# Kernel optimization log

Measured on AMD Instinct MI355X. Metric: run time of the kernel, lower is better.

Reference implementation:

```python
import jax, jax.numpy as jnp
import numpy as np

LAYERS, BLOCKS = 10, 4
RC, DC, SC, EC = 32, 32, 256, 256  # residual, dilation, skip, end channels
CIN, COUT, K = 6, 1, 2
DILATIONS = [2 ** (i % LAYERS) for i in range(BLOCKS * LAYERS)]
NL = len(DILATIONS)


def conv1d(x, w, dilation=1, pad=0):
    # x: [N, C, T], w: [O, I, K]
    return jax.lax.conv_general_dilated(
        x, w, window_strides=(1,), padding=[(pad, pad)],
        rhs_dilation=(dilation,), dimension_numbers=('NCH', 'OIH', 'NCH'))


def setup_inputs() -> dict:
    key = jax.random.key(0)
    ks = jax.random.split(key, 10)
    s = 0.1
    return {
        'x': jax.random.normal(ks[0], (8, CIN, 8192), dtype=jnp.float32),
        'start_w': jax.random.normal(ks[1], (RC, CIN, 1), dtype=jnp.float32) * s,
        'filter_w': jax.random.normal(ks[2], (NL, DC, RC, K), dtype=jnp.float32) * s,
        'gate_w': jax.random.normal(ks[3], (NL, DC, RC, K), dtype=jnp.float32) * s,
        'res_w': jax.random.normal(ks[4], (NL, RC, DC, 1), dtype=jnp.float32) * s,
        'skip_w': jax.random.normal(ks[5], (NL, SC, DC, 1), dtype=jnp.float32) * s,
        'end1_w': jax.random.normal(ks[6], (EC, SC, 1), dtype=jnp.float32) * s,
        'end1_b': jax.random.normal(ks[7], (EC,), dtype=jnp.float32) * s,
        'end2_w': jax.random.normal(ks[8], (COUT, EC, 1), dtype=jnp.float32) * s,
        'end2_b': jax.random.normal(ks[9], (COUT,), dtype=jnp.float32) * s,
    }


def reference(x, start_w, filter_w, gate_w, res_w, skip_w, end1_w, end1_b, end2_w, end2_b):
    x = conv1d(x, start_w)  # [B, RC, T]
    T = x.shape[2]
    # symmetric padding=(K-1)*d makes length grow by d each layer;
    # the shortest skip is the first one: T + (K-1)*DILATIONS[0]
    min_len = T + (K - 1) * DILATIONS[0]
    skip_sum = jnp.zeros((x.shape[0], SC, min_len), dtype=x.dtype)
    for i, d in enumerate(DILATIONS):
        pad = (K - 1) * d
        f = jnp.tanh(conv1d(x, filter_w[i], d, pad))
        g = jax.nn.sigmoid(conv1d(x, gate_w[i], d, pad))
        x = f * g  # [B, DC, T'] with T' = T_prev + d
        s = conv1d(x, skip_w[i])
        skip_sum = skip_sum + s[:, :, -min_len:]
        x = conv1d(x, res_w[i]) + x  # residual add (RC == DC)
    h = jax.nn.relu(skip_sum)
    h = jax.nn.relu(conv1d(h, end1_w) + end1_b[None, :, None])
    h = conv1d(h, end2_w) + end2_b[None, :, None]
    return h[:, :, -1]  # [B, COUT]
```

## Files before the change

kernel.cpp:

```cpp
#include <hip/hip_runtime.h>
#include <hip/hip_fp16.h>
#include <math.h>


#define NL 40
#define TLEN 8192

#define F_BLOB 0
#define F_C0   40960
#define F_Z    41216
#define F_H    51456
#define F_OB   53504
#define F_CNT  53512

typedef __attribute__((ext_vector_type(2))) _Float16 h2;

#if defined(__has_builtin)
#if __has_builtin(__builtin_amdgcn_fdot2)
#define HAS_FDOT2 1
#endif
#endif

__device__ __forceinline__ float FDOT2(h2 a, h2 b, float c) {
#ifdef HAS_FDOT2
    return __builtin_amdgcn_fdot2(a, b, c, false);
#else
    return c + (float)a.x * (float)b.x + (float)a.y * (float)b.y;
#endif
}

__device__ __forceinline__ float tanh_fast(float f) {
    f = fminf(fmaxf(f, -15.f), 15.f);
    float e2 = __expf(2.f * f);
    return (e2 - 1.f) / (e2 + 1.f);
}

__global__ __launch_bounds__(256) void k1_fold(
    const float* __restrict__ x, const float* __restrict__ start_w,
    const float* __restrict__ filter_w, const float* __restrict__ gate_w,
    const float* __restrict__ res_w, float* __restrict__ ws)
{
    const int l = blockIdx.x, m = blockIdx.y;
    const int t = threadIdx.x;

    if (l == NL) {
        if (m == 0) {
            const int b = t >> 5, ch = t & 31;
            float acc = 0.f;
#pragma unroll
            for (int j = 0; j < 6; ++j)
                acc += start_w[ch * 6 + j] * x[(b * 6 + j) * TLEN + TLEN - 1];
            ws[F_C0 + t] = acc;
            if (t < 8) { ws[F_OB + t] = 0.f; ((int*)(ws + F_CNT))[t] = 0; }
        } else {
            for (int k = t; k < 2048; k += 256) ws[F_H + k] = 0.f;
        }
        return;
    }

    __shared__ float F[32][32];
    __shared__ __align__(16) float R[32][36];
    const float* src = m ? gate_w : filter_w;
    for (int e = t; e < 1024; e += 256)
        F[e >> 5][e & 31] = src[(l * 1024 + e) * 2];
    if (l > 0)
        for (int e = t; e < 1024; e += 256) {
            const int k = e >> 5, j = e & 31;
            R[k][j] = res_w[(l - 1) * 1024 + e] + (k == j ? 1.f : 0.f);
        }
    __syncthreads();

    const int ch = t >> 3, jg = t & 7, j0 = jg * 4;
    float o0, o1, o2, o3;
    if (l == 0) {
        o0 = F[ch][j0]; o1 = F[ch][j0+1]; o2 = F[ch][j0+2]; o3 = F[ch][j0+3];
    } else {
        o0 = o1 = o2 = o3 = 0.f;
#pragma unroll
        for (int k = 0; k < 32; ++k) {
            const float fv = F[ch][k];
            const float4 rv = *(const float4*)&R[k][j0];
            o0 += fv * rv.x; o1 += fv * rv.y; o2 += fv * rv.z; o3 += fv * rv.w;
        }
    }
    const int hh = jg >> 2;
    __half* dst = (__half*)ws + (size_t)l * 2048 + (hh * 32 + ch) * 32
                + (m ? 16 : 0) + (j0 & 15);
    ((__half2*)dst)[0] = __floats2half2_rn(o0, o1);
    ((__half2*)dst)[1] = __floats2half2_rn(o2, o3);
}

#define K2_PREF(L, W) do {                                                   \
    if ((L) < NL) {                                                          \
        _Pragma("unroll")                                                    \
        for (int i = 0; i < 4; ++i)                                          \
            W[i] = blob[(L) * 256 + lane * 4 + i];                           \
    }                                                                        \
} while (0)

#define K2_STEP(L, W) do {                                                   \
    h2 s[8];                                                                 \
    { const float4* sp = (const float4*)zsm;                                 \
      *(float4*)&s[0] = sp[h * 2];                                           \
      *(float4*)&s[4] = sp[h * 2 + 1]; }                                     \
    float f = 0.f, g = 0.f;                                                  \
    const h2* wf = (const h2*)&W[0];                                         \
    const h2* wg = (const h2*)&W[2];                                         \
    _Pragma("unroll")                                                        \
    for (int i = 0; i < 8; ++i) {                                            \
        f = FDOT2(wf[i], s[i], f);                                           \
        g = FDOT2(wg[i], s[i], g);                                           \
    }                                                                        \
    f += __shfl_xor(f, 32, 64);                                              \
    g += __shfl_xor(g, 32, 64);                                              \
    float z = tanh_fast(f) * (1.f / (1.f + __expf(-g)));                     \
    if (h == 0) {                                                            \
        zbuf[((L) * 8 + b) * 32 + ch] = z;                                   \
        zsm[ch] = __float2half(z);                                           \
    }                                                                        \
    __builtin_amdgcn_wave_barrier();                                         \
    K2_PREF((L) + 4, W);                                                     \
} while (0)

__global__ __launch_bounds__(64) void k2_recur(float* __restrict__ ws)
{
    const int b = blockIdx.x;
    const int lane = threadIdx.x;
    const int ch = lane & 31, h = lane >> 5;
    __shared__ __align__(16) __half zsm[32];
    float* zbuf = ws + F_Z;

    if (h == 0) zsm[ch] = __float2half(ws[F_C0 + b * 32 + ch]);
    __builtin_amdgcn_wave_barrier();

    const float4* blob = (const float4*)ws;
    float4 w0[4], w1[4], w2[4], w3[4];
    K2_PREF(0, w0); K2_PREF(1, w1); K2_PREF(2, w2); K2_PREF(3, w3);
    for (int l = 0; l < NL; l += 4) {
        K2_STEP(l + 0, w0);
        K2_STEP(l + 1, w1);
        K2_STEP(l + 2, w2);
        K2_STEP(l + 3, w3);
    }
}

__global__ __launch_bounds__(256) void k3a_skip(
    const float* __restrict__ skip_w, float* __restrict__ ws)
{
    const int l = blockIdx.x, b = blockIdx.y, t = threadIdx.x;
    __shared__ __align__(16) float zsm[32];
    if (t < 32) zsm[t] = ws[F_Z + (l * 8 + b) * 32 + t];
    __syncthreads();
    const float4* w4 = (const float4*)(skip_w + (size_t)(l * 256 + t) * 32);
    const float4* z4 = (const float4*)zsm;
    float acc = 0.f;
#pragma unroll
    for (int i = 0; i < 8; ++i) {
        float4 wv = w4[i], zv = z4[i];
        acc += wv.x*zv.x + wv.y*zv.y + wv.z*zv.z + wv.w*zv.w;
    }
    atomicAdd(&ws[F_H + b * 256 + t], acc);
}

__global__ __launch_bounds__(256) void k3b_end(
    const float* __restrict__ end1_w, const float* __restrict__ end1_b,
    const float* __restrict__ end2_w, const float* __restrict__ end2_b,
    float* __restrict__ ws, float* __restrict__ out)
{
    const int q = blockIdx.x, b = blockIdx.y, t = threadIdx.x;
    __shared__ __align__(16) float hsm[256];
    __shared__ float psum[64][5];
    const int p = t >> 6, oc = t & 63, row = q * 64 + oc;

    float4 wreg[16];
    const float4* wp = (const float4*)(end1_w + (size_t)row * 256 + p * 64);
#pragma unroll
    for (int i = 0; i < 16; ++i) wreg[i] = wp[i];

    hsm[t] = fmaxf(ws[F_H + b * 256 + t], 0.f);
    __syncthreads();
    const float4* h4 = (const float4*)(hsm + p * 64);
    float acc = 0.f;
#pragma unroll
    for (int i = 0; i < 16; ++i) {
        float4 wv = wreg[i], hv = h4[i];
        acc += wv.x*hv.x + wv.y*hv.y + wv.z*hv.z + wv.w*hv.w;
    }
    psum[oc][p] = acc;
    __syncthreads();
    if (t < 64) {
        const int rr = q * 64 + t;
        float e = psum[t][0] + psum[t][1] + psum[t][2] + psum[t][3]
                + end1_b[rr];
        e = fmaxf(e, 0.f);
        float pe = e * end2_w[rr];
#pragma unroll
        for (int off = 32; off > 0; off >>= 1)
            pe += __shfl_down(pe, off, 64);
        if (t == 0) {
            float* obuf = ws + F_OB;
            int* cnt = (int*)(ws + F_CNT);
            atomicAdd(&obuf[b], pe);
            __threadfence();
            int old = __hip_atomic_fetch_add(&cnt[b], 1, __ATOMIC_ACQ_REL,
                                             __HIP_MEMORY_SCOPE_AGENT);
            if (old == 3) {
                float tot = __hip_atomic_load(&obuf[b], __ATOMIC_ACQUIRE,
                                              __HIP_MEMORY_SCOPE_AGENT);
                out[b] = tot + end2_b[0];
            }
        }
    }
}

extern "C" void kernel_launch(void* const* d_in, const int* in_sizes, int n_in,
                              void* d_out, int out_size, void* d_ws, size_t ws_size,
                              hipStream_t stream) {
    const float* x        = (const float*)d_in[0];
    const float* start_w  = (const float*)d_in[1];
    const float* filter_w = (const float*)d_in[2];
    const float* gate_w   = (const float*)d_in[3];
    const float* res_w    = (const float*)d_in[4];
    const float* skip_w   = (const float*)d_in[5];
    const float* end1_w   = (const float*)d_in[6];
    const float* end1_b   = (const float*)d_in[7];
    const float* end2_w   = (const float*)d_in[8];
    const float* end2_b   = (const float*)d_in[9];
    float* out = (float*)d_out;
    float* ws  = (float*)d_ws;

    k1_fold <<<dim3(NL + 1, 2), 256, 0, stream>>>(x, start_w, filter_w,
                                                  gate_w, res_w, ws);
    k2_recur<<<8, 64, 0, stream>>>(ws);
    k3a_skip<<<dim3(NL, 8), 256, 0, stream>>>(skip_w, ws);
    k3b_end <<<dim3(4, 8), 256, 0, stream>>>(end1_w, end1_b, end2_w, end2_b,
                                             ws, out);
}
```

Before: 98.52 us.

## Fuse four kernels into one persistent kernel with atomic counter dependencies

Merges the fold, recurrence, skip and end kernels into a single 161-block launch, with global atomic counters and spin-waits replacing kernel boundaries. Downstream blocks prefetch their weights into registers before waiting, so those loads overlap the upstream stages. The skip stage now handles all 8 batches per layer block, reusing the skip weights across batches. The sync counters are zeroed with a memset before the launch. This removes several launch gaps in exchange for spin-wait overhead, and it relies on every block being co-resident, otherwise it can deadlock.

```diff
diff --git a/kernel.cpp b/kernel.cpp
--- a/kernel.cpp
+++ b/kernel.cpp
@@ -10,8 +10,9 @@
 #define F_C0   40960
 #define F_Z    41216
 #define F_H    51456
-#define F_OB   53504
-#define F_CNT  53512
+#define F_SYNC 53504
+#define SYNC_BYTE_OFF (F_SYNC * 4)
+#define SYNC_BYTES 96
 
 typedef __attribute__((ext_vector_type(2))) _Float16 h2;
 
@@ -35,59 +36,13 @@
     return (e2 - 1.f) / (e2 + 1.f);
 }
 
-__global__ __launch_bounds__(256) void k1_fold(
-    const float* __restrict__ x, const float* __restrict__ start_w,
-    const float* __restrict__ filter_w, const float* __restrict__ gate_w,
-    const float* __restrict__ res_w, float* __restrict__ ws)
-{
-    const int l = blockIdx.x, m = blockIdx.y;
-    const int t = threadIdx.x;
-
-    if (l == NL) {
-        if (m == 0) {
-            const int b = t >> 5, ch = t & 31;
-            float acc = 0.f;
-#pragma unroll
-            for (int j = 0; j < 6; ++j)
-                acc += start_w[ch * 6 + j] * x[(b * 6 + j) * TLEN + TLEN - 1];
-            ws[F_C0 + t] = acc;
-            if (t < 8) { ws[F_OB + t] = 0.f; ((int*)(ws + F_CNT))[t] = 0; }
-        } else {
-            for (int k = t; k < 2048; k += 256) ws[F_H + k] = 0.f;
-        }
-        return;
-    }
-
-    __shared__ float F[32][32];
-    __shared__ __align__(16) float R[32][36];
-    const float* src = m ? gate_w : filter_w;
-    for (int e = t; e < 1024; e += 256)
-        F[e >> 5][e & 31] = src[(l * 1024 + e) * 2];
-    if (l > 0)
-        for (int e = t; e < 1024; e += 256) {
-            const int k = e >> 5, j = e & 31;
-            R[k][j] = res_w[(l - 1) * 1024 + e] + (k == j ? 1.f : 0.f);
-        }
-    __syncthreads();
-
-    const int ch = t >> 3, jg = t & 7, j0 = jg * 4;
-    float o0, o1, o2, o3;
-    if (l == 0) {
-        o0 = F[ch][j0]; o1 = F[ch][j0+1]; o2 = F[ch][j0+2]; o3 = F[ch][j0+3];
-    } else {
-        o0 = o1 = o2 = o3 = 0.f;
-#pragma unroll
-        for (int k = 0; k < 32; ++k) {
-            const float fv = F[ch][k];
-            const float4 rv = *(const float4*)&R[k][j0];
-            o0 += fv * rv.x; o1 += fv * rv.y; o2 += fv * rv.z; o3 += fv * rv.w;
-        }
-    }
-    const int hh = jg >> 2;
-    __half* dst = (__half*)ws + (size_t)l * 2048 + (hh * 32 + ch) * 32
-                + (m ? 16 : 0) + (j0 & 15);
-    ((__half2*)dst)[0] = __floats2half2_rn(o0, o1);
-    ((__half2*)dst)[1] = __floats2half2_rn(o2, o3);
+__device__ __forceinline__ void rel_cnt(int* p) {
+    __hip_atomic_fetch_add(p, 1, __ATOMIC_ACQ_REL, __HIP_MEMORY_SCOPE_AGENT);
+}
+__device__ __forceinline__ void wait_cnt(const int* p, int target) {
+    while (__hip_atomic_load(p, __ATOMIC_ACQUIRE, __HIP_MEMORY_SCOPE_AGENT)
+           < target)
+        __builtin_amdgcn_s_sleep(8);
 }
 
 #define K2_PREF(L, W) do {                                                   \
@@ -104,110 +59,177 @@
       *(float4*)&s[0] = sp[h * 2];                                           \
       *(float4*)&s[4] = sp[h * 2 + 1]; }                                     \
     float f = 0.f, g = 0.f;                                                  \
-    const h2* wf = (const h2*)&W[0];                                         \
-    const h2* wg = (const h2*)&W[2];                                         \
+    const h2* wfp = (const h2*)&W[0];                                        \
+    const h2* wgp = (const h2*)&W[2];                                        \
     _Pragma("unroll")                                                        \
     for (int i = 0; i < 8; ++i) {                                            \
-        f = FDOT2(wf[i], s[i], f);                                           \
-        g = FDOT2(wg[i], s[i], g);                                           \
+        f = FDOT2(wfp[i], s[i], f);                                          \
+        g = FDOT2(wgp[i], s[i], g);                                          \
     }                                                                        \
     f += __shfl_xor(f, 32, 64);                                              \
     g += __shfl_xor(g, 32, 64);                                              \
     float z = tanh_fast(f) * (1.f / (1.f + __expf(-g)));                     \
     if (h == 0) {                                                            \
-        zbuf[((L) * 8 + b) * 32 + ch] = z;                                   \
+        zbuf[(L) * 256 + b * 32 + ch] = z;                                   \
         zsm[ch] = __float2half(z);                                           \
     }                                                                        \
     __builtin_amdgcn_wave_barrier();                                         \
     K2_PREF((L) + 4, W);                                                     \
 } while (0)
 
-__global__ __launch_bounds__(64) void k2_recur(float* __restrict__ ws)
-{
-    const int b = blockIdx.x;
-    const int lane = threadIdx.x;
-    const int ch = lane & 31, h = lane >> 5;
-    __shared__ __align__(16) __half zsm[32];
-    float* zbuf = ws + F_Z;
-
-    if (h == 0) zsm[ch] = __float2half(ws[F_C0 + b * 32 + ch]);
-    __builtin_amdgcn_wave_barrier();
-
-    const float4* blob = (const float4*)ws;
-    float4 w0[4], w1[4], w2[4], w3[4];
-    K2_PREF(0, w0); K2_PREF(1, w1); K2_PREF(2, w2); K2_PREF(3, w3);
-    for (int l = 0; l < NL; l += 4) {
-        K2_STEP(l + 0, w0);
-        K2_STEP(l + 1, w1);
-        K2_STEP(l + 2, w2);
-        K2_STEP(l + 3, w3);
-    }
-}
-
-__global__ __launch_bounds__(256) void k3a_skip(
-    const float* __restrict__ skip_w, float* __restrict__ ws)
-{
-    const int l = blockIdx.x, b = blockIdx.y, t = threadIdx.x;
-    __shared__ __align__(16) float zsm[32];
-    if (t < 32) zsm[t] = ws[F_Z + (l * 8 + b) * 32 + t];
-    __syncthreads();
-    const float4* w4 = (const float4*)(skip_w + (size_t)(l * 256 + t) * 32);
-    const float4* z4 = (const float4*)zsm;
-    float acc = 0.f;
-#pragma unroll
-    for (int i = 0; i < 8; ++i) {
-        float4 wv = w4[i], zv = z4[i];
-        acc += wv.x*zv.x + wv.y*zv.y + wv.z*zv.z + wv.w*zv.w;
-    }
-    atomicAdd(&ws[F_H + b * 256 + t], acc);
-}
-
-__global__ __launch_bounds__(256) void k3b_end(
+__global__ __launch_bounds__(256) void wavenet_mega(
+    const float* __restrict__ x, const float* __restrict__ start_w,
+    const float* __restrict__ filter_w, const float* __restrict__ gate_w,
+    const float* __restrict__ res_w, const float* __restrict__ skip_w,
     const float* __restrict__ end1_w, const float* __restrict__ end1_b,
     const float* __restrict__ end2_w, const float* __restrict__ end2_b,
     float* __restrict__ ws, float* __restrict__ out)
 {
-    const int q = blockIdx.x, b = blockIdx.y, t = threadIdx.x;
-    __shared__ __align__(16) float hsm[256];
-    __shared__ float psum[64][5];
-    const int p = t >> 6, oc = t & 63, row = q * 64 + oc;
-
-    float4 wreg[16];
-    const float4* wp = (const float4*)(end1_w + (size_t)row * 256 + p * 64);
-#pragma unroll
-    for (int i = 0; i < 16; ++i) wreg[i] = wp[i];
-
-    hsm[t] = fmaxf(ws[F_H + b * 256 + t], 0.f);
-    __syncthreads();
-    const float4* h4 = (const float4*)(hsm + p * 64);
-    float acc = 0.f;
-#pragma unroll
-    for (int i = 0; i < 16; ++i) {
-        float4 wv = wreg[i], hv = h4[i];
-        acc += wv.x*hv.x + wv.y*hv.y + wv.z*hv.z + wv.w*hv.w;
-    }
-    psum[oc][p] = acc;
-    __syncthreads();
-    if (t < 64) {
-        const int rr = q * 64 + t;
-        float e = psum[t][0] + psum[t][1] + psum[t][2] + psum[t][3]
-                + end1_b[rr];
-        e = fmaxf(e, 0.f);
-        float pe = e * end2_w[rr];
-#pragma unroll
-        for (int off = 32; off > 0; off >>= 1)
-            pe += __shfl_down(pe, off, 64);
-        if (t == 0) {
-            float* obuf = ws + F_OB;
-            int* cnt = (int*)(ws + F_CNT);
-            atomicAdd(&obuf[b], pe);
-            __threadfence();
-            int old = __hip_atomic_fetch_add(&cnt[b], 1, __ATOMIC_ACQ_REL,
-                                             __HIP_MEMORY_SCOPE_AGENT);
-            if (old == 3) {
-                float tot = __hip_atomic_load(&obuf[b], __ATOMIC_ACQUIRE,
-                                              __HIP_MEMORY_SCOPE_AGENT);
-                out[b] = tot + end2_b[0];
+    const int id = blockIdx.x, t = threadIdx.x;
+    int*   cnt1 = (int*)(ws + F_SYNC);
+    int*   cnt2 = cnt1 + 1;
+    int*   cnt3 = cnt1 + 2;
+    float* obuf = ws + F_SYNC + 8;
+    int*   cnt4 = (int*)(ws + F_SYNC + 16);
+    float* zbuf = ws + F_Z;
+    float* hsum = ws + F_H;
+
+    if (id < 80) {
+        const int l = id >> 1, m = id & 1;
+        __shared__ float F[32][32];
+        __shared__ __align__(16) float R[32][36];
+        const float* src = m ? gate_w : filter_w;
+        for (int e = t; e < 1024; e += 256)
+            F[e >> 5][e & 31] = src[(l * 1024 + e) * 2];
+        if (l > 0)
+            for (int e = t; e < 1024; e += 256) {
+                const int k = e >> 5, j = e & 31;
+                R[k][j] = res_w[(l - 1) * 1024 + e] + (k == j ? 1.f : 0.f);
+            }
+        __syncthreads();
+        const int ch = t >> 3, jg = t & 7, j0 = jg * 4;
+        float o0, o1, o2, o3;
+        if (l == 0) {
+            o0 = F[ch][j0]; o1 = F[ch][j0+1]; o2 = F[ch][j0+2]; o3 = F[ch][j0+3];
+        } else {
+            o0 = o1 = o2 = o3 = 0.f;
+#pragma unroll
+            for (int k = 0; k < 32; ++k) {
+                const float fv = F[ch][k];
+                const float4 rv = *(const float4*)&R[k][j0];
+                o0 += fv*rv.x; o1 += fv*rv.y; o2 += fv*rv.z; o3 += fv*rv.w;
+            }
+        }
+        const int hh = jg >> 2;
+        __half* dst = (__half*)ws + (size_t)l * 2048 + (hh * 32 + ch) * 32
+                    + (m ? 16 : 0) + (j0 & 15);
+        ((__half2*)dst)[0] = __floats2half2_rn(o0, o1);
+        ((__half2*)dst)[1] = __floats2half2_rn(o2, o3);
+        __syncthreads();
+        if (t == 0) rel_cnt(cnt1);
+    }
+    else if (id == 80) {
+        const int b = t >> 5, ch = t & 31;
+        float acc = 0.f;
+#pragma unroll
+        for (int j = 0; j < 6; ++j)
+            acc += start_w[ch * 6 + j] * x[(b * 6 + j) * TLEN + TLEN - 1];
+        ws[F_C0 + t] = acc;
+#pragma unroll
+        for (int k = t; k < 2048; k += 256) hsum[k] = 0.f;
+        __syncthreads();
+        if (t == 0) rel_cnt(cnt1);
+    }
+    else if (id < 89) {
+        if (t >= 64) return;
+        const int b = id - 81;
+        const int lane = t;
+        const int ch = lane & 31, h = lane >> 5;
+        __shared__ __align__(16) __half zsm[32];
+
+        wait_cnt(cnt1, 81);
+
+        if (h == 0) zsm[ch] = __float2half(ws[F_C0 + b * 32 + ch]);
+        __builtin_amdgcn_wave_barrier();
+
+        const float4* blob = (const float4*)ws;
+        float4 w0[4], w1[4], w2[4], w3[4];
+        K2_PREF(0, w0); K2_PREF(1, w1); K2_PREF(2, w2); K2_PREF(3, w3);
+        for (int l = 0; l < NL; l += 4) {
+            K2_STEP(l + 0, w0);
+            K2_STEP(l + 1, w1);
+            K2_STEP(l + 2, w2);
+            K2_STEP(l + 3, w3);
+        }
+        if (lane == 0) rel_cnt(cnt2);
+    }
+    else if (id < 129) {
+        const int l = id - 89;
+        __shared__ __align__(16) float zsm[256];
+        float4 wreg[8];
+        const float4* wp = (const float4*)(skip_w + (size_t)(l * 256 + t) * 32);
+#pragma unroll
+        for (int i = 0; i < 8; ++i) wreg[i] = wp[i];
+
+        wait_cnt(cnt2, 8);
+        zsm[t] = zbuf[l * 256 + t];
+        __syncthreads();
+#pragma unroll
+        for (int b = 0; b < 8; ++b) {
+            const float4* z4 = (const float4*)(zsm + b * 32);
+            float acc = 0.f;
+#pragma unroll
+            for (int i = 0; i < 8; ++i) {
+                float4 wv = wreg[i], zv = z4[i];
+                acc += wv.x*zv.x + wv.y*zv.y + wv.z*zv.z + wv.w*zv.w;
+            }
+            atomicAdd(&hsum[b * 256 + t], acc);
+        }
+        __syncthreads();
+        if (t == 0) rel_cnt(cnt3);
+    }
+    else {
+        const int e = id - 129, b = e >> 2, q = e & 3;
+        const int p = t >> 6, oc = t & 63, row = q * 64 + oc;
+        __shared__ __align__(16) float hsm[256];
+        __shared__ float psum[64][5];
+
+        float4 wreg[16];
+        const float4* wp = (const float4*)(end1_w + (size_t)row * 256 + p * 64);
+#pragma unroll
+        for (int i = 0; i < 16; ++i) wreg[i] = wp[i];
+
+        wait_cnt(cnt3, 40);
+        hsm[t] = fmaxf(hsum[b * 256 + t], 0.f);
+        __syncthreads();
+        const float4* h4 = (const float4*)(hsm + p * 64);
+        float acc = 0.f;
+#pragma unroll
+        for (int i = 0; i < 16; ++i) {
+            float4 wv = wreg[i], hv = h4[i];
+            acc += wv.x*hv.x + wv.y*hv.y + wv.z*hv.z + wv.w*hv.w;
+        }
+        psum[oc][p] = acc;
+        __syncthreads();
+        if (t < 64) {
+            const int rr = q * 64 + t;
+            float ev = psum[t][0] + psum[t][1] + psum[t][2] + psum[t][3]
+                     + end1_b[rr];
+            ev = fmaxf(ev, 0.f);
+            float pe = ev * end2_w[rr];
+#pragma unroll
+            for (int off = 32; off > 0; off >>= 1)
+                pe += __shfl_down(pe, off, 64);
+            if (t == 0) {
+                atomicAdd(&obuf[b], pe);
+                __threadfence();
+                int old = __hip_atomic_fetch_add(&cnt4[b], 1, __ATOMIC_ACQ_REL,
+                                                 __HIP_MEMORY_SCOPE_AGENT);
+                if (old == 3) {
+                    float tot = __hip_atomic_load(&obuf[b], __ATOMIC_ACQUIRE,
+                                                  __HIP_MEMORY_SCOPE_AGENT);
+                    out[b] = tot + end2_b[0];
+                }
             }
         }
     }
@@ -229,10 +251,8 @@
     float* out = (float*)d_out;
     float* ws  = (float*)d_ws;
 
-    k1_fold <<<dim3(NL + 1, 2), 256, 0, stream>>>(x, start_w, filter_w,
-                                                  gate_w, res_w, ws);
-    k2_recur<<<8, 64, 0, stream>>>(ws);
-    k3a_skip<<<dim3(NL, 8), 256, 0, stream>>>(skip_w, ws);
-    k3b_end <<<dim3(4, 8), 256, 0, stream>>>(end1_w, end1_b, end2_w, end2_b,
-                                             ws, out);
-}
+    hipMemsetAsync((char*)d_ws + SYNC_BYTE_OFF, 0, SYNC_BYTES, stream);
+    wavenet_mega<<<161, 256, 0, stream>>>(
+        x, start_w, filter_w, gate_w, res_w, skip_w,
+        end1_w, end1_b, end2_w, end2_b, ws, out);
+}
```

Measured after the change: 123.9 us. +25.8%, slower.

## Fuse skip and end convolutions into recurrence kernel with fp16 weight prep

Applied to the files above, without the earlier changes.

Launches four kernels as two. The prep kernel now also converts the skip and end1 weights to fp16 in a transposed layout. A single per-batch kernel runs the gated recurrence on wave 0, while four extra waves accumulate skip contributions from a shared ring buffer one layer behind, then compute the end MLP in-block. This removes the atomics, zero-init, cross-block counter and two launches, at the cost of a block-wide sync every layer and fp16 precision for the skip and end1 weights.

```diff
diff --git a/kernel.cpp b/kernel.cpp
--- a/kernel.cpp
+++ b/kernel.cpp
@@ -6,12 +6,10 @@
 #define NL 40
 #define TLEN 8192
 
-#define F_BLOB 0
-#define F_C0   40960
-#define F_Z    41216
-#define F_H    51456
-#define F_OB   53504
-#define F_CNT  53512
+#define F_BLOBFG 0
+#define F_BLOBSK 40960
+#define F_BLOBE1 204800
+#define F_C0     237568
 
 typedef __attribute__((ext_vector_type(2))) _Float16 h2;
 
@@ -35,182 +33,191 @@
     return (e2 - 1.f) / (e2 + 1.f);
 }
 
-__global__ __launch_bounds__(256) void k1_fold(
+__global__ __launch_bounds__(256) void k1_prep(
     const float* __restrict__ x, const float* __restrict__ start_w,
     const float* __restrict__ filter_w, const float* __restrict__ gate_w,
-    const float* __restrict__ res_w, float* __restrict__ ws)
+    const float* __restrict__ res_w, const float* __restrict__ skip_w,
+    const float* __restrict__ end1_w, float* __restrict__ ws)
 {
-    const int l = blockIdx.x, m = blockIdx.y;
-    const int t = threadIdx.x;
-
-    if (l == NL) {
-        if (m == 0) {
-            const int b = t >> 5, ch = t & 31;
-            float acc = 0.f;
-#pragma unroll
-            for (int j = 0; j < 6; ++j)
-                acc += start_w[ch * 6 + j] * x[(b * 6 + j) * TLEN + TLEN - 1];
-            ws[F_C0 + t] = acc;
-            if (t < 8) { ws[F_OB + t] = 0.f; ((int*)(ws + F_CNT))[t] = 0; }
+    const int id = blockIdx.x, t = threadIdx.x;
+
+    if (id < 80) {
+        const int l = id >> 1, m = id & 1;
+        __shared__ float F[32][32];
+        __shared__ __align__(16) float R[32][36];
+        const float* src = m ? gate_w : filter_w;
+        for (int e = t; e < 1024; e += 256)
+            F[e >> 5][e & 31] = src[(l * 1024 + e) * 2];
+        if (l > 0)
+            for (int e = t; e < 1024; e += 256) {
+                const int k = e >> 5, j = e & 31;
+                R[k][j] = res_w[(l - 1) * 1024 + e] + (k == j ? 1.f : 0.f);
+            }
+        __syncthreads();
+        const int ch = t >> 3, jg = t & 7, j0 = jg * 4;
+        float o0, o1, o2, o3;
+        if (l == 0) {
+            o0 = F[ch][j0]; o1 = F[ch][j0+1]; o2 = F[ch][j0+2]; o3 = F[ch][j0+3];
         } else {
-            for (int k = t; k < 2048; k += 256) ws[F_H + k] = 0.f;
+            o0 = o1 = o2 = o3 = 0.f;
+#pragma unroll
+            for (int k = 0; k < 32; ++k) {
+                const float fv = F[ch][k];
+                const float4 rv = *(const float4*)&R[k][j0];
+                o0 += fv*rv.x; o1 += fv*rv.y; o2 += fv*rv.z; o3 += fv*rv.w;
+            }
         }
-        return;
-    }
-
-    __shared__ float F[32][32];
-    __shared__ __align__(16) float R[32][36];
-    const float* src = m ? gate_w : filter_w;
-    for (int e = t; e < 1024; e += 256)
-        F[e >> 5][e & 31] = src[(l * 1024 + e) * 2];
-    if (l > 0)
-        for (int e = t; e < 1024; e += 256) {
-            const int k = e >> 5, j = e & 31;
-            R[k][j] = res_w[(l - 1) * 1024 + e] + (k == j ? 1.f : 0.f);
+        const int hh = jg >> 2;
+        __half* dst = (__half*)ws + (size_t)l * 2048 + (hh * 32 + ch) * 32
+                    + (m ? 16 : 0) + (j0 & 15);
+        ((__half2*)dst)[0] = __floats2half2_rn(o0, o1);
+        ((__half2*)dst)[1] = __floats2half2_rn(o2, o3);
+    }
+    else if (id == 80) {
+        const int b = t >> 5, ch = t & 31;
+        float acc = 0.f;
+#pragma unroll
+        for (int j = 0; j < 6; ++j)
+            acc += start_w[ch * 6 + j] * x[(b * 6 + j) * TLEN + TLEN - 1];
+        ws[F_C0 + t] = acc;
+    }
+    else if (id < 241) {
+        const int q = (id - 81) * 256 + t;
+        const float4* s4 = (const float4*)skip_w;
+        const float4 a = s4[q * 2], bb = s4[q * 2 + 1];
+        __half2* d = (__half2*)(ws + F_BLOBSK);
+        d[q * 4 + 0] = __floats2half2_rn(a.x,  a.y);
+        d[q * 4 + 1] = __floats2half2_rn(a.z,  a.w);
+        d[q * 4 + 2] = __floats2half2_rn(bb.x, bb.y);
+        d[q * 4 + 3] = __floats2half2_rn(bb.z, bb.w);
+    }
+    else {
+        __half2* d = (__half2*)(ws + F_BLOBE1);
+#pragma unroll
+        for (int k = 0; k < 2; ++k) {
+            const int dd = (id - 241) * 512 + k * 256 + t;
+            const int ec = dd & 255, sc2 = dd >> 8;
+            const float v0 = end1_w[ec * 256 + 2 * sc2];
+            const float v1 = end1_w[ec * 256 + 2 * sc2 + 1];
+            d[dd] = __floats2half2_rn(v0, v1);
         }
-    __syncthreads();
-
-    const int ch = t >> 3, jg = t & 7, j0 = jg * 4;
-    float o0, o1, o2, o3;
-    if (l == 0) {
-        o0 = F[ch][j0]; o1 = F[ch][j0+1]; o2 = F[ch][j0+2]; o3 = F[ch][j0+3];
-    } else {
-        o0 = o1 = o2 = o3 = 0.f;
-#pragma unroll
-        for (int k = 0; k < 32; ++k) {
-            const float fv = F[ch][k];
-            const float4 rv = *(const float4*)&R[k][j0];
-            o0 += fv * rv.x; o1 += fv * rv.y; o2 += fv * rv.z; o3 += fv * rv.w;
-        }
-    }
-    const int hh = jg >> 2;
-    __half* dst = (__half*)ws + (size_t)l * 2048 + (hh * 32 + ch) * 32
-                + (m ? 16 : 0) + (j0 & 15);
-    ((__half2*)dst)[0] = __floats2half2_rn(o0, o1);
-    ((__half2*)dst)[1] = __floats2half2_rn(o2, o3);
-}
-
-#define K2_PREF(L, W) do {                                                   \
+    }
+}
+
+#define PF(L, W) do {                                                        \
     if ((L) < NL) {                                                          \
         _Pragma("unroll")                                                    \
         for (int i = 0; i < 4; ++i)                                          \
-            W[i] = blob[(L) * 256 + lane * 4 + i];                           \
+            W[i] = blobfg[(L) * 256 + lane * 4 + i];                         \
     }                                                                        \
 } while (0)
 
-#define K2_STEP(L, W) do {                                                   \
-    h2 s[8];                                                                 \
-    { const float4* sp = (const float4*)zsm;                                 \
-      *(float4*)&s[0] = sp[h * 2];                                           \
-      *(float4*)&s[4] = sp[h * 2 + 1]; }                                     \
-    float f = 0.f, g = 0.f;                                                  \
-    const h2* wf = (const h2*)&W[0];                                         \
-    const h2* wg = (const h2*)&W[2];                                         \
-    _Pragma("unroll")                                                        \
-    for (int i = 0; i < 8; ++i) {                                            \
-        f = FDOT2(wf[i], s[i], f);                                           \
-        g = FDOT2(wg[i], s[i], g);                                           \
+#define SPF(L, SW) do {                                                      \
+    if ((L) < NL) {                                                          \
+        _Pragma("unroll")                                                    \
+        for (int i = 0; i < 4; ++i)                                          \
+            SW[i] = blobsk[(L) * 1024 + sc * 4 + i];                         \
     }                                                                        \
-    f += __shfl_xor(f, 32, 64);                                              \
-    g += __shfl_xor(g, 32, 64);                                              \
-    float z = tanh_fast(f) * (1.f / (1.f + __expf(-g)));                     \
-    if (h == 0) {                                                            \
-        zbuf[((L) * 8 + b) * 32 + ch] = z;                                   \
-        zsm[ch] = __float2half(z);                                           \
+} while (0)
+
+#define BODY(L, FG, SW) do {                                                 \
+    if (wv == 0) {                                                           \
+        h2 s[8];                                                             \
+        { const float4* sp = (const float4*)zown;                            \
+          *(float4*)&s[0] = sp[h * 2];                                       \
+          *(float4*)&s[4] = sp[h * 2 + 1]; }                                 \
+        float f = 0.f, g = 0.f;                                              \
+        const h2* wfp = (const h2*)&FG[0];                                   \
+        const h2* wgp = (const h2*)&FG[2];                                   \
+        _Pragma("unroll")                                                    \
+        for (int i = 0; i < 8; ++i) {                                        \
+            f = FDOT2(wfp[i], s[i], f);                                      \
+            g = FDOT2(wgp[i], s[i], g);                                      \
+        }                                                                    \
+        f += __shfl_xor(f, 32, 64);                                          \
+        g += __shfl_xor(g, 32, 64);                                          \
+        const float z = tanh_fast(f) * (1.f / (1.f + __expf(-g)));           \
+        const __half hz = __float2half(z);                                   \
+        if (h == 0) { zown[ch] = hz; zring[(L) & 1][ch] = hz; }              \
+        PF((L) + 4, FG);                                                     \
+    } else {                                                                 \
+        if ((L) >= 1) {                                                      \
+            const h2* zr2 = (const h2*)zring[((L) - 1) & 1];                 \
+            const h2* wp  = (const h2*)SW;                                   \
+            _Pragma("unroll")                                                \
+            for (int i = 0; i < 16; ++i)                                     \
+                skip_acc = FDOT2(wp[i], zr2[i], skip_acc);                   \
+        }                                                                    \
+        SPF((L) + 1, SW);                                                    \
     }                                                                        \
-    __builtin_amdgcn_wave_barrier();                                         \
-    K2_PREF((L) + 4, W);                                                     \
+    __syncthreads();                                                         \
 } while (0)
 
-__global__ __launch_bounds__(64) void k2_recur(float* __restrict__ ws)
+__global__ __launch_bounds__(320) void k2_all(
+    const float* __restrict__ end1_b, const float* __restrict__ end2_w,
+    const float* __restrict__ end2_b, const float* __restrict__ ws,
+    float* __restrict__ out)
 {
-    const int b = blockIdx.x;
-    const int lane = threadIdx.x;
+    const int b = blockIdx.x, t = threadIdx.x;
+    const int wv = t >> 6, lane = t & 63;
     const int ch = lane & 31, h = lane >> 5;
-    __shared__ __align__(16) __half zsm[32];
-    float* zbuf = ws + F_Z;
-
-    if (h == 0) zsm[ch] = __float2half(ws[F_C0 + b * 32 + ch]);
-    __builtin_amdgcn_wave_barrier();
-
-    const float4* blob = (const float4*)ws;
-    float4 w0[4], w1[4], w2[4], w3[4];
-    K2_PREF(0, w0); K2_PREF(1, w1); K2_PREF(2, w2); K2_PREF(3, w3);
+    const int sc = t - 64;
+
+    __shared__ __align__(16) __half zown[32];
+    __shared__ __align__(16) __half zring[2][32];
+    __shared__ __align__(16) __half hhalf[256];
+    __shared__ float psum[4];
+
+    const float4* blobfg = (const float4*)ws;
+    const float4* blobsk = (const float4*)(ws + F_BLOBSK);
+    const h2*     blobe1 = (const h2*)(ws + F_BLOBE1);
+
+    float4 fg0[4], fg1[4], fg2[4], fg3[4];
+    float4 sw0[4], sw1[4];
+    float skip_acc = 0.f, b1 = 0.f, w2 = 0.f;
+
+    if (wv == 0) {
+        if (h == 0) zown[ch] = __float2half(ws[F_C0 + b * 32 + ch]);
+        PF(0, fg0); PF(1, fg1); PF(2, fg2); PF(3, fg3);
+    } else {
+        b1 = end1_b[sc];
+        w2 = end2_w[sc];
+        SPF(0, sw0);
+    }
+    __syncthreads();
+
     for (int l = 0; l < NL; l += 4) {
-        K2_STEP(l + 0, w0);
-        K2_STEP(l + 1, w1);
-        K2_STEP(l + 2, w2);
-        K2_STEP(l + 3, w3);
-    }
-}
-
-__global__ __launch_bounds__(256) void k3a_skip(
-    const float* __restrict__ skip_w, float* __restrict__ ws)
-{
-    const int l = blockIdx.x, b = blockIdx.y, t = threadIdx.x;
-    __shared__ __align__(16) float zsm[32];
-    if (t < 32) zsm[t] = ws[F_Z + (l * 8 + b) * 32 + t];
+        BODY(l + 0, fg0, sw1);
+        BODY(l + 1, fg1, sw0);
+        BODY(l + 2, fg2, sw1);
+        BODY(l + 3, fg3, sw0);
+    }
+
+    if (wv >= 1) {
+        const h2* zr2 = (const h2*)zring[1];
+        const h2* wp  = (const h2*)sw1;
+#pragma unroll
+        for (int i = 0; i < 16; ++i)
+            skip_acc = FDOT2(wp[i], zr2[i], skip_acc);
+        hhalf[sc] = __float2half(fmaxf(skip_acc, 0.f));
+    }
     __syncthreads();
-    const float4* w4 = (const float4*)(skip_w + (size_t)(l * 256 + t) * 32);
-    const float4* z4 = (const float4*)zsm;
-    float acc = 0.f;
-#pragma unroll
-    for (int i = 0; i < 8; ++i) {
-        float4 wv = w4[i], zv = z4[i];
-        acc += wv.x*zv.x + wv.y*zv.y + wv.z*zv.z + wv.w*zv.w;
-    }
-    atomicAdd(&ws[F_H + b * 256 + t], acc);
-}
-
-__global__ __launch_bounds__(256) void k3b_end(
-    const float* __restrict__ end1_w, const float* __restrict__ end1_b,
-    const float* __restrict__ end2_w, const float* __restrict__ end2_b,
-    float* __restrict__ ws, float* __restrict__ out)
-{
-    const int q = blockIdx.x, b = blockIdx.y, t = threadIdx.x;
-    __shared__ __align__(16) float hsm[256];
-    __shared__ float psum[64][5];
-    const int p = t >> 6, oc = t & 63, row = q * 64 + oc;
-
-    float4 wreg[16];
-    const float4* wp = (const float4*)(end1_w + (size_t)row * 256 + p * 64);
-#pragma unroll
-    for (int i = 0; i < 16; ++i) wreg[i] = wp[i];
-
-    hsm[t] = fmaxf(ws[F_H + b * 256 + t], 0.f);
-    __syncthreads();
-    const float4* h4 = (const float4*)(hsm + p * 64);
-    float acc = 0.f;
-#pragma unroll
-    for (int i = 0; i < 16; ++i) {
-        float4 wv = wreg[i], hv = h4[i];
-        acc += wv.x*hv.x + wv.y*hv.y + wv.z*hv.z + wv.w*hv.w;
-    }
-    psum[oc][p] = acc;
-    __syncthreads();
-    if (t < 64) {
-        const int rr = q * 64 + t;
-        float e = psum[t][0] + psum[t][1] + psum[t][2] + psum[t][3]
-                + end1_b[rr];
-        e = fmaxf(e, 0.f);
-        float pe = e * end2_w[rr];
+
+    if (wv >= 1) {
+        float acc = b1;
+        const h2* hh2 = (const h2*)hhalf;
+#pragma unroll 8
+        for (int s2 = 0; s2 < 128; ++s2)
+            acc = FDOT2(blobe1[s2 * 256 + sc], hh2[s2], acc);
+        float pe = fmaxf(acc, 0.f) * w2;
 #pragma unroll
         for (int off = 32; off > 0; off >>= 1)
             pe += __shfl_down(pe, off, 64);
-        if (t == 0) {
-            float* obuf = ws + F_OB;
-            int* cnt = (int*)(ws + F_CNT);
-            atomicAdd(&obuf[b], pe);
-            __threadfence();
-            int old = __hip_atomic_fetch_add(&cnt[b], 1, __ATOMIC_ACQ_REL,
-                                             __HIP_MEMORY_SCOPE_AGENT);
-            if (old == 3) {
-                float tot = __hip_atomic_load(&obuf[b], __ATOMIC_ACQUIRE,
-                                              __HIP_MEMORY_SCOPE_AGENT);
-                out[b] = tot + end2_b[0];
-            }
-        }
-    }
+        if (lane == 0) psum[wv - 1] = pe;
+    }
+    __syncthreads();
+    if (t == 64)
+        out[b] = psum[0] + psum[1] + psum[2] + psum[3] + end2_b[0];
 }
 
 extern "C" void kernel_launch(void* const* d_in, const int* in_sizes, int n_in,
@@ -229,10 +236,7 @@
     float* out = (float*)d_out;
     float* ws  = (float*)d_ws;
 
-    k1_fold <<<dim3(NL + 1, 2), 256, 0, stream>>>(x, start_w, filter_w,
-                                                  gate_w, res_w, ws);
-    k2_recur<<<8, 64, 0, stream>>>(ws);
-    k3a_skip<<<dim3(NL, 8), 256, 0, stream>>>(skip_w, ws);
-    k3b_end <<<dim3(4, 8), 256, 0, stream>>>(end1_w, end1_b, end2_w, end2_b,
-                                             ws, out);
-}
+    k1_prep<<<305, 256, 0, stream>>>(x, start_w, filter_w, gate_w, res_w,
+                                     skip_w, end1_w, ws);
+    k2_all <<<8, 320, 0, stream>>>(end1_b, end2_w, end2_b, ws, out);
+}
```

New measurement: 106.9 us. 1.08x slower.
